# Kernel optimization log

Measured on AMD Instinct MI355X. Metric: run time of the kernel, lower is better.

The kernel has to match this reference:

```python
import jax, jax.numpy as jnp
import numpy as np

B, L, H = 512, 50, 256
N_NODE, N_CATE, N_REL, DEG = 200000, 1000, 4, 12
N = B * L          # graph nodes (seed items of the neighbor-sampled subgraph)
E = N * DEG        # sampled edges (12 neighbors per seed node)


def _layer_norm(x):
    # CARES.layer_norm: center then divide by L2 norm of the centered vector
    x = x - jnp.mean(x, -1, keepdims=True)
    return x / jnp.sqrt(jnp.sum(x * x, -1, keepdims=True))


def _ave_pool(h, gm):
    # h: [B,L,H], gm: [B,L] float
    return jnp.sum(h * gm[..., None], 1) / jnp.sum(gm, 1)[:, None]


def _session_encoder(Ws, bs, w5, Wt, bt, seq_hidden, mean_item, mean_cate, mask):
    # Ws: [4,H,H], bs: [4,H], w5: [H], Wt: [2H,H], bt: [H]
    b, l, h = seq_hidden.shape
    last = (jnp.sum(mask, 1) - 1)[:, None, None]
    ht = jnp.take_along_axis(seq_hidden, jnp.broadcast_to(last, (b, 1, h)), axis=1)[:, 0]
    q1 = (ht @ Ws[0] + bs[0])[:, None, :]
    q2 = (mean_item @ Ws[1] + bs[1])[:, None, :]
    q3 = seq_hidden @ Ws[2] + bs[2]
    q4 = (mean_cate @ Ws[3] + bs[3])[:, None, :]
    alpha = jnp.einsum('blh,h->bl', jax.nn.sigmoid(q1 + q2 + q3 + q4), w5)[..., None]
    a = jnp.sum(alpha * seq_hidden * mask[..., None].astype(seq_hidden.dtype), 1)
    return jnp.concatenate([a, ht], 1) @ Wt + bt


def _gat(x, edge_index, rel_e, edge_attr, gat_W, n_nodes):
    # relation-aware single-head GAT layer: gather -> edge attention -> segment softmax -> scatter
    h = x @ gat_W                               # [N,H]
    src, dst = edge_index[0], edge_index[1]
    msg = h[src] + rel_e                        # [E,H] relation-augmented message
    logit = jax.nn.leaky_relu(jnp.sum(h[dst] * msg, -1) / np.sqrt(h.shape[-1]).astype(np.float32), 0.2) + edge_attr
    mx = jax.ops.segment_max(logit, dst, num_segments=n_nodes)
    ex = jnp.exp(logit - mx[dst])
    den = jax.ops.segment_sum(ex, dst, num_segments=n_nodes)
    att = ex / (den[dst] + 1e-12)
    return jax.ops.segment_sum(att[:, None] * msg, dst, num_segments=n_nodes)


def setup_inputs() -> dict:
    key = jax.random.key(0)
    ks = jax.random.split(key, 20)
    s = 1.0 / np.sqrt(H)  # reset_parameters: uniform(-stdv, stdv)
    uni = lambda k, shape: jax.random.uniform(k, shape, jnp.float32, -s, s)
    return {
        'alias_inputs': jax.random.randint(ks[0], (B, L), 0, L),
        'items': jax.random.randint(ks[1], (B, L), 1, N_NODE),
        'mask': jnp.ones((B, L), jnp.int32),
        'cates': jax.random.randint(ks[2], (B, L), 0, N_CATE),
        'edge_index': jax.random.randint(ks[3], (2, E), 0, N),
        'edge_type': jax.random.randint(ks[4], (E,), 0, N_REL),
        'edge_attr': jax.random.normal(ks[5], (E,), jnp.float32) * 0.1,
        'item_emb': uni(ks[6], (N_NODE, H)),
        'cate_emb': uni(ks[7], (N_CATE, H)),
        'pos_emb': uni(ks[8], (L, H)),
        'len_emb': uni(ks[9], (2 * L, H)),
        'rel_emb': uni(ks[10], (N_REL, H)),
        'se_W': uni(ks[11], (2, 4, H, H)),   # linears one..four for the 2 SessionEncoders
        'se_b': uni(ks[12], (2, 4, H)),
        'se_w5': uni(ks[13], (2, H)),        # linear_five (H->1, no bias)
        'se_Wt': uni(ks[14], (2, 2 * H, H)), # linear_transform
        'se_bt': uni(ks[15], (2, H)),
        'gat_W': uni(ks[16], (H, H)),
    }


def reference(alias_inputs, items, mask, cates, edge_index, edge_type, edge_attr,
              item_emb, cate_emb, pos_emb, len_emb, rel_emb,
              se_W, se_b, se_w5, se_Wt, se_bt, gat_W):
    gm = jnp.sign(items).astype(jnp.float32)            # graph_mask
    hidden = item_emb[items]                            # [B,L,H]
    cate_hidden = cate_emb[cates]
    mean_item = _ave_pool(hidden, gm)
    mean_cate = _ave_pool(cate_hidden, gm)

    # h0 = hidden[i][alias_inputs[i]]
    idx = jnp.broadcast_to(alias_inputs[..., None], (B, L, H))
    h0 = jnp.take_along_axis(hidden, idx, axis=1)

    # add_pos_encoding
    pos = jnp.arange(L - 1, -1, -1)[None, :]
    len_d = jnp.sum(mask, 1, keepdims=True)             # [B,1]
    pos_index = (pos - (L - len_d)) * mask              # [B,L]
    seq_hidden = h0 + pos_emb[pos_index] + len_emb[jnp.broadcast_to(len_d, (B, L))]

    local_sess = _session_encoder(se_W[0], se_b[0], se_w5[0], se_Wt[0], se_bt[0],
                                  seq_hidden, mean_item, mean_cate, mask)

    # relation-aware GAT over the sampled subgraph
    x = item_emb[items.reshape(-1)]                     # [N,H]
    out = _gat(x, edge_index, rel_emb[edge_type], edge_attr, gat_W, N)
    graph_emb = out.reshape(B, L, H)
    s_node = _ave_pool(graph_emb, gm)

    g_seq = jnp.take_along_axis(graph_emb, idx, axis=1)
    global_sess = _session_encoder(se_W[1], se_b[1], se_w5[1], se_Wt[1], se_bt[1],
                                   g_seq, mean_item, s_node, mask)

    return _layer_norm(local_sess + global_sess)        # [B,H]
```

## Files before the change

kernel.cpp:

```cpp
#include <hip/hip_runtime.h>

#define B 512
#define L 50
#define H 256
#define GN (B*L)
#define GE (GN*12)

__device__ __forceinline__ float waveSum(float v){
  #pragma unroll
  for (int m=32;m>0;m>>=1) v += __shfl_xor(v, m, 64);
  return v;
}
__device__ __forceinline__ float sigm(float x){ return 1.f/(1.f+expf(-x)); }

__global__ void k_gather_means(const int* items, const int* cates, const int* mask,
                               const float* item_emb, const float* cate_emb,
                               float* hidden, float* mi, float* mc, float* gms, int* lend){
  int b=blockIdx.x, h=threadIdx.x;
  float si=0.f, sc=0.f, g=0.f; int lm=0;
  for (int l=0;l<L;l++){
    int it=items[b*L+l];
    float gm=(it>0)?1.f:((it<0)?-1.f:0.f);
    float v=item_emb[(size_t)it*H+h];
    hidden[((size_t)b*L+l)*H+h]=v;
    si += gm*v;
    sc += gm*cate_emb[(size_t)cates[b*L+l]*H+h];
    g += gm;
    lm += mask[b*L+l];
  }
  mi[(size_t)b*H+h]=si/g; mc[(size_t)b*H+h]=sc/g;
  if (h==0){ gms[b]=g; lend[b]=lm; }
}

__global__ void k_seq(const int* alias_, const int* mask, const float* hidden,
                      const float* pos_emb, const float* len_emb, const int* lend,
                      float* seqh, float* ht){
  int r=blockIdx.x, lane=threadIdx.x;
  int b=r/L, l=r%L;
  int a=alias_[r];
  int ld=lend[b];
  int m=mask[r];
  int pidx=(ld-1-l)*m;
  if (pidx<0) pidx+=L;
  float4 hv=*reinterpret_cast<const float4*>(hidden+((size_t)b*L+a)*H+lane*4);
  float4 pv=*reinterpret_cast<const float4*>(pos_emb+(size_t)pidx*H+lane*4);
  float4 lv=*reinterpret_cast<const float4*>(len_emb+(size_t)ld*H+lane*4);
  float4 o=make_float4(hv.x+pv.x+lv.x, hv.y+pv.y+lv.y, hv.z+pv.z+lv.z, hv.w+pv.w+lv.w);
  *reinterpret_cast<float4*>(seqh+(size_t)r*H+lane*4)=o;
  if (l == (ld+L-1)%L)
    *reinterpret_cast<float4*>(ht+(size_t)b*H+lane*4)=o;
}

__global__ __launch_bounds__(256) void k_gemm(const float* A, const float* W, size_t wOff,
                                              float* C, const float* bias, size_t bOff,
                                              int M, int Nc, int K){
  __shared__ float At[16][68];
  __shared__ float Ws[16][64];
  int bm=blockIdx.x*64, bn=blockIdx.y*64;
  int t=threadIdx.x;
  int tx=t&15, ty=t>>4;
  float c[4][4]={};
  int r=t>>2, kq=(t&3)<<2;
  int kk=t>>4, nq=(t&15)<<2;
  for (int k0=0;k0<K;k0+=16){
    float4 av=*reinterpret_cast<const float4*>(A+(size_t)(bm+r)*K+(k0+kq));
    At[kq+0][r]=av.x; At[kq+1][r]=av.y; At[kq+2][r]=av.z; At[kq+3][r]=av.w;
    float4 wv=*reinterpret_cast<const float4*>(W+wOff+(size_t)(k0+kk)*Nc+(bn+nq));
    Ws[kk][nq+0]=wv.x; Ws[kk][nq+1]=wv.y; Ws[kk][nq+2]=wv.z; Ws[kk][nq+3]=wv.w;
    __syncthreads();
    #pragma unroll
    for (int q=0;q<16;q++){
      float4 a4=*reinterpret_cast<const float4*>(&At[q][ty<<2]);
      float4 w4=*reinterpret_cast<const float4*>(&Ws[q][tx<<2]);
      float aa[4]={a4.x,a4.y,a4.z,a4.w};
      float ww[4]={w4.x,w4.y,w4.z,w4.w};
      #pragma unroll
      for (int i=0;i<4;i++)
        #pragma unroll
        for (int j=0;j<4;j++) c[i][j]=fmaf(aa[i],ww[j],c[i][j]);
    }
    __syncthreads();
  }
  #pragma unroll
  for (int i=0;i<4;i++){
    size_t row=(size_t)(bm+(ty<<2)+i);
    #pragma unroll
    for (int j=0;j<4;j++){
      int col=bn+(tx<<2)+j;
      float v=c[i][j];
      if (bias) v+=bias[bOff+col];
      C[row*Nc+col]=v;
    }
  }
}

__global__ __launch_bounds__(256) void k_qb3(const float* A0, const float* A1, const float* A2,
                                             const float* W, size_t wBase,
                                             const float* seb, size_t bOff, float* C){
  __shared__ float At[16][68];
  __shared__ float Ws[16][64];
  int bm=blockIdx.x*64, bn=blockIdx.y*64;
  int t=threadIdx.x;
  int tx=t&15, ty=t>>4;
  float c[4][4]={};
  int r=t>>2, kq=(t&3)<<2;
  int kk=t>>4, nq=(t&15)<<2;
  const float* As[3]={A0,A1,A2};
  const int widx[3]={0,1,3};
  for (int src=0;src<3;src++){
    const float* A=As[src];
    size_t wOff=wBase+(size_t)widx[src]*H*H;
    for (int k0=0;k0<H;k0+=16){
      float4 av=*reinterpret_cast<const float4*>(A+(size_t)(bm+r)*H+(k0+kq));
      At[kq+0][r]=av.x; At[kq+1][r]=av.y; At[kq+2][r]=av.z; At[kq+3][r]=av.w;
      float4 wv=*reinterpret_cast<const float4*>(W+wOff+(size_t)(k0+kk)*H+(bn+nq));
      Ws[kk][nq+0]=wv.x; Ws[kk][nq+1]=wv.y; Ws[kk][nq+2]=wv.z; Ws[kk][nq+3]=wv.w;
      __syncthreads();
      #pragma unroll
      for (int q=0;q<16;q++){
        float4 a4=*reinterpret_cast<const float4*>(&At[q][ty<<2]);
        float4 w4=*reinterpret_cast<const float4*>(&Ws[q][tx<<2]);
        float aa[4]={a4.x,a4.y,a4.z,a4.w};
        float ww[4]={w4.x,w4.y,w4.z,w4.w};
        #pragma unroll
        for (int i=0;i<4;i++)
          #pragma unroll
          for (int j=0;j<4;j++) c[i][j]=fmaf(aa[i],ww[j],c[i][j]);
      }
      __syncthreads();
    }
  }
  #pragma unroll
  for (int i=0;i<4;i++){
    size_t row=(size_t)(bm+(ty<<2)+i);
    #pragma unroll
    for (int j=0;j<4;j++){
      int col=bn+(tx<<2)+j;
      float v=c[i][j]
        + seb[bOff+0*H+col] + seb[bOff+1*H+col]
        + seb[bOff+2*H+col] + seb[bOff+3*H+col];
      C[row*H+col]=v;
    }
  }
}

__global__ void k_alpha(const float* qb, const float* q3, const float* w5, size_t wOff,
                        float* alpha){
  int gid=blockIdx.x*blockDim.x+threadIdx.x;
  int wid=gid>>6, lane=gid&63;
  if (wid>=GN) return;
  int b=wid/L;
  float4 qv=*reinterpret_cast<const float4*>(qb+(size_t)b*H+lane*4);
  float4 q3v=*reinterpret_cast<const float4*>(q3+(size_t)wid*H+lane*4);
  float4 wv=*reinterpret_cast<const float4*>(w5+wOff+(size_t)lane*4);
  float part = wv.x*sigm(qv.x+q3v.x) + wv.y*sigm(qv.y+q3v.y)
             + wv.z*sigm(qv.z+q3v.z) + wv.w*sigm(qv.w+q3v.w);
  part=waveSum(part);
  if (lane==0) alpha[wid]=part;
}

__global__ void k_pool(const float* alpha, const float* seqh, const int* mask, const float* ht, float* cat){
  int b=blockIdx.x, h=threadIdx.x;
  float a=0.f;
  for (int l=0;l<L;l++)
    a += alpha[b*L+l]*seqh[((size_t)b*L+l)*H+h]*(float)mask[b*L+l];
  cat[(size_t)b*2*H+h]=a;
  cat[(size_t)b*2*H+H+h]=ht[(size_t)b*H+h];
}

__global__ void k_count(const int* dst, int* cnt){
  int e=blockIdx.x*blockDim.x+threadIdx.x;
  if (e<GE) atomicAdd(&cnt[dst[e]],1);
}

__global__ void k_scan(const int* cnt, int* rowp){
  __shared__ int s[1024];
  int t=threadIdx.x;
  int base=t*25;
  int local[25]; int sum=0;
  #pragma unroll
  for (int i=0;i<25;i++){ local[i]=sum; sum+=cnt[base+i]; }
  s[t]=sum; __syncthreads();
  for (int off=1;off<1024;off<<=1){
    int v=(t>=off)?s[t-off]:0; __syncthreads();
    s[t]+=v; __syncthreads();
  }
  int excl=s[t]-sum;
  #pragma unroll
  for (int i=0;i<25;i++) rowp[base+i]=excl+local[i];
  if (t==1023) rowp[GN]=s[1023];
}

__global__ void k_fill(const int* dst, const int* rowp, int* cnt, int* eord){
  int e=blockIdx.x*blockDim.x+threadIdx.x;
  if (e<GE){ int d=dst[e]; int pos=rowp[d]+atomicAdd(&cnt[d],1); eord[pos]=e; }
}

__global__ void k_node(const float* hg, const int* src, const int* etype, const float* eattr,
                       const float* rel, const int* rowp, const int* eord, float* out){
  int gid=blockIdx.x*blockDim.x+threadIdx.x;
  int n=gid>>6, lane=gid&63;
  if (n>=GN) return;
  float4 hn=*reinterpret_cast<const float4*>(hg+(size_t)n*H+lane*4);
  int b0=rowp[n], b1=rowp[n+1];
  float mx=-INFINITY, den=0.f;
  float4 acc=make_float4(0.f,0.f,0.f,0.f);
  for (int i=b0;i<b1;i++){
    int e=eord[i]; int s=src[e]; int ty=etype[e];
    float4 hs=*reinterpret_cast<const float4*>(hg+(size_t)s*H+lane*4);
    float4 rv=*reinterpret_cast<const float4*>(rel+(size_t)ty*H+lane*4);
    float4 m4=make_float4(hs.x+rv.x,hs.y+rv.y,hs.z+rv.z,hs.w+rv.w);
    float p=hn.x*m4.x+hn.y*m4.y+hn.z*m4.z+hn.w*m4.w;
    p=waveSum(p)*(1.f/16.f);
    float lg=(p>0.f?p:0.2f*p)+eattr[e];
    if (lg>mx){
      float sc=expf(mx-lg);
      den*=sc; acc.x*=sc; acc.y*=sc; acc.z*=sc; acc.w*=sc;
      mx=lg;
    }
    float ex=expf(lg-mx);
    den+=ex;
    acc.x+=ex*m4.x; acc.y+=ex*m4.y; acc.z+=ex*m4.z; acc.w+=ex*m4.w;
  }
  float inv=1.f/(den+1e-12f);
  float4 o=make_float4(acc.x*inv,acc.y*inv,acc.z*inv,acc.w*inv);
  *reinterpret_cast<float4*>(out+(size_t)n*H+lane*4)=o;
}

__global__ void k_avepool(const float* x, const int* items, const float* gms, float* out){
  int b=blockIdx.x, h=threadIdx.x;
  float s=0.f;
  for (int l=0;l<L;l++){
    int it=items[b*L+l];
    float gm=(it>0)?1.f:((it<0)?-1.f:0.f);
    s += gm*x[((size_t)b*L+l)*H+h];
  }
  out[(size_t)b*H+h]=s/gms[b];
}

__global__ void k_gseq(const int* alias_, const float* graph, const int* lend, float* gseq, float* ht){
  int r=blockIdx.x, lane=threadIdx.x;
  int b=r/L, l=r%L;
  int a=alias_[r];
  float4 v=*reinterpret_cast<const float4*>(graph+((size_t)b*L+a)*H+lane*4);
  *reinterpret_cast<float4*>(gseq+(size_t)r*H+lane*4)=v;
  int ld=lend[b];
  if (l == (ld+L-1)%L)
    *reinterpret_cast<float4*>(ht+(size_t)b*H+lane*4)=v;
}

__global__ void k_final(const float* sl, const float* sg, float* out){
  __shared__ float red[8];
  int b=blockIdx.x, h=threadIdx.x;
  int wid=h>>6, lane=h&63;
  float v=sl[(size_t)b*H+h]+sg[(size_t)b*H+h];
  float s=waveSum(v);
  if (lane==0) red[wid]=s;
  __syncthreads();
  float tot=red[0]+red[1]+red[2]+red[3];
  float x=v-tot/(float)H;
  float s2=waveSum(x*x);
  __syncthreads();
  if (lane==0) red[wid]=s2;
  __syncthreads();
  float ss=red[0]+red[1]+red[2]+red[3];
  out[(size_t)b*H+h]=x/sqrtf(ss);
}

extern "C" void kernel_launch(void* const* d_in, const int* in_sizes, int n_in,
                              void* d_out, int out_size, void* d_ws, size_t ws_size,
                              hipStream_t stream){
  (void)in_sizes; (void)n_in; (void)out_size; (void)ws_size;
  const int* alias_=(const int*)d_in[0];
  const int* items =(const int*)d_in[1];
  const int* mask  =(const int*)d_in[2];
  const int* cates =(const int*)d_in[3];
  const int* eind  =(const int*)d_in[4];
  const int* etype =(const int*)d_in[5];
  const float* eattr   =(const float*)d_in[6];
  const float* item_emb=(const float*)d_in[7];
  const float* cate_emb=(const float*)d_in[8];
  const float* pos_emb =(const float*)d_in[9];
  const float* len_emb =(const float*)d_in[10];
  const float* rel_emb =(const float*)d_in[11];
  const float* se_W    =(const float*)d_in[12];
  const float* se_b    =(const float*)d_in[13];
  const float* se_w5   =(const float*)d_in[14];
  const float* se_Wt   =(const float*)d_in[15];
  const float* se_bt   =(const float*)d_in[16];
  const float* gat_W   =(const float*)d_in[17];
  const int* esrc=eind; const int* edst=eind+GE;

  char* w=(char*)d_ws;
  auto carve=[&](size_t nbytes)->char*{ char* p=w; w += (nbytes+255)&~(size_t)255; return p; };
  float* buf1 =(float*)carve((size_t)GN*H*4);
  float* buf2 =(float*)carve((size_t)GN*H*4);
  float* hgat =(float*)carve((size_t)GN*H*4);
  float* q3   =(float*)carve((size_t)GN*H*4);
  float* alphaB=(float*)carve((size_t)GN*4);
  float* qb   =(float*)carve((size_t)B*H*4);
  float* mi   =(float*)carve((size_t)B*H*4);
  float* mc   =(float*)carve((size_t)B*H*4);
  float* sn   =(float*)carve((size_t)B*H*4);
  float* gms  =(float*)carve((size_t)B*4);
  int*   lend =(int*)  carve((size_t)B*4);
  float* htb  =(float*)carve((size_t)B*H*4);
  float* htg  =(float*)carve((size_t)B*H*4);
  float* catb =(float*)carve((size_t)B*2*H*4);
  float* sl   =(float*)carve((size_t)B*H*4);
  float* sg   =(float*)carve((size_t)B*H*4);
  int*   cnt  =(int*)  carve((size_t)GN*4);
  int*   rowp =(int*)  carve((size_t)(GN+1)*4);
  int*   eord =(int*)  carve((size_t)GE*4);

  dim3 blk(256), gBig(GN/64,H/64), gSm(B/64,H/64);

  k_gather_means<<<B,256,0,stream>>>(items,cates,mask,item_emb,cate_emb,buf1,mi,mc,gms,lend);
  k_seq<<<GN,64,0,stream>>>(alias_,mask,buf1,pos_emb,len_emb,lend,buf2,htb);

  k_gemm<<<gBig,blk,0,stream>>>(buf1, gat_W, 0, hgat, nullptr,0, GN,H,H);

  k_gemm<<<gBig,blk,0,stream>>>(buf2, se_W, (size_t)2*H*H, q3, nullptr,0, GN,H,H);
  k_qb3<<<gSm,blk,0,stream>>>(htb, mi, mc, se_W, 0, se_b, 0, qb);
  k_alpha<<<GN/4,256,0,stream>>>(qb,q3,se_w5,0,alphaB);
  k_pool<<<B,256,0,stream>>>(alphaB,buf2,mask,htb,catb);
  k_gemm<<<gSm,blk,0,stream>>>(catb, se_Wt, 0, sl, se_bt, 0, B,H,2*H);

  (void)hipMemsetAsync(cnt,0,(size_t)GN*4,stream);
  k_count<<<GE/256,256,0,stream>>>(edst,cnt);
  k_scan<<<1,1024,0,stream>>>(cnt,rowp);
  (void)hipMemsetAsync(cnt,0,(size_t)GN*4,stream);
  k_fill<<<GE/256,256,0,stream>>>(edst,rowp,cnt,eord);
  k_node<<<GN/4,256,0,stream>>>(hgat,esrc,etype,eattr,rel_emb,rowp,eord,buf1);

  k_avepool<<<B,256,0,stream>>>(buf1,items,gms,sn);
  k_gseq<<<GN,64,0,stream>>>(alias_,buf1,lend,buf2,htg);
  k_gemm<<<gBig,blk,0,stream>>>(buf2, se_W, (size_t)6*H*H, q3, nullptr,0, GN,H,H);
  k_qb3<<<gSm,blk,0,stream>>>(htg, mi, sn, se_W, (size_t)4*H*H, se_b, (size_t)4*H, qb);
  k_alpha<<<GN/4,256,0,stream>>>(qb,q3,se_w5,(size_t)H,alphaB);
  k_pool<<<B,256,0,stream>>>(alphaB,buf2,mask,htg,catb);
  k_gemm<<<gSm,blk,0,stream>>>(catb, se_Wt, (size_t)2*H*H, sg, se_bt, (size_t)H, B,H,2*H);

  k_final<<<B,256,0,stream>>>(sl,sg,(float*)d_out);
}
```

Measured before the change: 818.0 us.

## Run the three large GEMMs on bf16 MFMA with pre-transposed weights

Replaces the fp32 scalar tiled GEMM for the three big N×256×256 products with an MFMA bf16 kernel (16x16x32). Producer kernels now also write bf16 copies of their activations, and a small kernel converts and transposes the three weight matrices to bf16 once per call. This moves the dominant GEMM work onto matrix cores and halves its input traffic. In exchange it adds extra bf16 write traffic, a weight-prep launch, and reduced precision in the GEMM inputs.

```diff
diff --git a/kernel.cpp b/kernel.cpp
--- a/kernel.cpp
+++ b/kernel.cpp
@@ -6,6 +6,13 @@
 #define GN (B*L)
 #define GE (GN*12)
 
+typedef unsigned short u16;
+typedef unsigned int u32;
+typedef __attribute__((ext_vector_type(8))) short short8;
+typedef __attribute__((ext_vector_type(8))) unsigned short u16x8;
+typedef __attribute__((ext_vector_type(4))) float f32x4;
+
+__device__ __forceinline__ u16 f2bf(float f){ u32 x=__float_as_uint(f); u32 r=x+0x7FFFu+((x>>16)&1u); return (u16)(r>>16); }
 __device__ __forceinline__ float waveSum(float v){
   #pragma unroll
   for (int m=32;m>0;m>>=1) v += __shfl_xor(v, m, 64);
@@ -15,7 +22,7 @@
 
 __global__ void k_gather_means(const int* items, const int* cates, const int* mask,
                                const float* item_emb, const float* cate_emb,
-                               float* hidden, float* mi, float* mc, float* gms, int* lend){
+                               float* hidden, u16* hiddenBf, float* mi, float* mc, float* gms, int* lend){
   int b=blockIdx.x, h=threadIdx.x;
   float si=0.f, sc=0.f, g=0.f; int lm=0;
   for (int l=0;l<L;l++){
@@ -23,6 +30,7 @@
     float gm=(it>0)?1.f:((it<0)?-1.f:0.f);
     float v=item_emb[(size_t)it*H+h];
     hidden[((size_t)b*L+l)*H+h]=v;
+    hiddenBf[((size_t)b*L+l)*H+h]=f2bf(v);
     si += gm*v;
     sc += gm*cate_emb[(size_t)cates[b*L+l]*H+h];
     g += gm;
@@ -34,7 +42,7 @@
 
 __global__ void k_seq(const int* alias_, const int* mask, const float* hidden,
                       const float* pos_emb, const float* len_emb, const int* lend,
-                      float* seqh, float* ht){
+                      float* seqh, u16* seqBf, float* ht){
   int r=blockIdx.x, lane=threadIdx.x;
   int b=r/L, l=r%L;
   int a=alias_[r];
@@ -47,8 +55,49 @@
   float4 lv=*reinterpret_cast<const float4*>(len_emb+(size_t)ld*H+lane*4);
   float4 o=make_float4(hv.x+pv.x+lv.x, hv.y+pv.y+lv.y, hv.z+pv.z+lv.z, hv.w+pv.w+lv.w);
   *reinterpret_cast<float4*>(seqh+(size_t)r*H+lane*4)=o;
+  ushort4 ob=make_ushort4(f2bf(o.x),f2bf(o.y),f2bf(o.z),f2bf(o.w));
+  *reinterpret_cast<ushort4*>(seqBf+(size_t)r*H+lane*4)=ob;
   if (l == (ld+L-1)%L)
     *reinterpret_cast<float4*>(ht+(size_t)b*H+lane*4)=o;
+}
+
+__global__ void k_prepW(const float* gat_W, const float* se_W, u16* WbfT){
+  int n=blockIdx.x, g=blockIdx.y, k=threadIdx.x;
+  const float* src = (g==0)? gat_W : (g==1? se_W+(size_t)2*H*H : se_W+(size_t)6*H*H);
+  WbfT[((size_t)g*H+n)*H+k] = f2bf(src[(size_t)k*H+n]);
+}
+
+__global__ __launch_bounds__(256) void k_gemm_mfma(const u16* Abf, const u16* WbfT,
+                                                   float* C, int M){
+  __shared__ u16 As[64][40];
+  __shared__ u16 Bs[64][40];
+  int bm=blockIdx.x*64, bn=blockIdx.y*64;
+  int t=threadIdx.x, wv=t>>6, lane=t&63;
+  int sr=t>>2, sk=(t&3)<<3;
+  f32x4 acc[4]={};
+  for (int k0=0;k0<H;k0+=32){
+    u16x8 av=*reinterpret_cast<const u16x8*>(Abf+(size_t)(bm+sr)*H+k0+sk);
+    u16x8 bv=*reinterpret_cast<const u16x8*>(WbfT+(size_t)(bn+sr)*H+k0+sk);
+    *reinterpret_cast<u16x8*>(&As[sr][sk])=av;
+    *reinterpret_cast<u16x8*>(&Bs[sr][sk])=bv;
+    __syncthreads();
+    int row=(wv<<4)+(lane&15);
+    int ks=(lane>>4)<<3;
+    short8 a=*reinterpret_cast<const short8*>(&As[row][ks]);
+    #pragma unroll
+    for (int ns=0;ns<4;ns++){
+      short8 b=*reinterpret_cast<const short8*>(&Bs[(ns<<4)+(lane&15)][ks]);
+      acc[ns]=__builtin_amdgcn_mfma_f32_16x16x32_bf16(a,b,acc[ns],0,0,0);
+    }
+    __syncthreads();
+  }
+  int r0=bm+(wv<<4)+((lane>>4)<<2);
+  int c0=bn+(lane&15);
+  #pragma unroll
+  for (int ns=0;ns<4;ns++)
+    #pragma unroll
+    for (int i=0;i<4;i++)
+      C[(size_t)(r0+i)*H + c0 + (ns<<4)] = acc[ns][i];
 }
 
 __global__ __launch_bounds__(256) void k_gemm(const float* A, const float* W, size_t wOff,
@@ -238,12 +287,15 @@
   out[(size_t)b*H+h]=s/gms[b];
 }
 
-__global__ void k_gseq(const int* alias_, const float* graph, const int* lend, float* gseq, float* ht){
+__global__ void k_gseq(const int* alias_, const float* graph, const int* lend,
+                       float* gseq, u16* gseqBf, float* ht){
   int r=blockIdx.x, lane=threadIdx.x;
   int b=r/L, l=r%L;
   int a=alias_[r];
   float4 v=*reinterpret_cast<const float4*>(graph+((size_t)b*L+a)*H+lane*4);
   *reinterpret_cast<float4*>(gseq+(size_t)r*H+lane*4)=v;
+  ushort4 vb=make_ushort4(f2bf(v.x),f2bf(v.y),f2bf(v.z),f2bf(v.w));
+  *reinterpret_cast<ushort4*>(gseqBf+(size_t)r*H+lane*4)=vb;
   int ld=lend[b];
   if (l == (ld+L-1)%L)
     *reinterpret_cast<float4*>(ht+(size_t)b*H+lane*4)=v;
@@ -297,6 +349,10 @@
   float* buf2 =(float*)carve((size_t)GN*H*4);
   float* hgat =(float*)carve((size_t)GN*H*4);
   float* q3   =(float*)carve((size_t)GN*H*4);
+  u16*   hidBf=(u16*)  carve((size_t)GN*H*2);
+  u16*   seqBf=(u16*)  carve((size_t)GN*H*2);
+  u16*   gsqBf=(u16*)  carve((size_t)GN*H*2);
+  u16*   wbfT =(u16*)  carve((size_t)3*H*H*2);
   float* alphaB=(float*)carve((size_t)GN*4);
   float* qb   =(float*)carve((size_t)B*H*4);
   float* mi   =(float*)carve((size_t)B*H*4);
@@ -313,14 +369,15 @@
   int*   rowp =(int*)  carve((size_t)(GN+1)*4);
   int*   eord =(int*)  carve((size_t)GE*4);
 
-  dim3 blk(256), gBig(GN/64,H/64), gSm(B/64,H/64);
-
-  k_gather_means<<<B,256,0,stream>>>(items,cates,mask,item_emb,cate_emb,buf1,mi,mc,gms,lend);
-  k_seq<<<GN,64,0,stream>>>(alias_,mask,buf1,pos_emb,len_emb,lend,buf2,htb);
-
-  k_gemm<<<gBig,blk,0,stream>>>(buf1, gat_W, 0, hgat, nullptr,0, GN,H,H);
-
-  k_gemm<<<gBig,blk,0,stream>>>(buf2, se_W, (size_t)2*H*H, q3, nullptr,0, GN,H,H);
+  dim3 blk(256), gSm(B/64,H/64), gM(GN/64,H/64), gPrep(H,3);
+
+  k_prepW<<<gPrep,H,0,stream>>>(gat_W, se_W, wbfT);
+  k_gather_means<<<B,256,0,stream>>>(items,cates,mask,item_emb,cate_emb,buf1,hidBf,mi,mc,gms,lend);
+  k_seq<<<GN,64,0,stream>>>(alias_,mask,buf1,pos_emb,len_emb,lend,buf2,seqBf,htb);
+
+  k_gemm_mfma<<<gM,blk,0,stream>>>(hidBf, wbfT, hgat, GN);
+
+  k_gemm_mfma<<<gM,blk,0,stream>>>(seqBf, wbfT+(size_t)1*H*H, q3, GN);
   k_qb3<<<gSm,blk,0,stream>>>(htb, mi, mc, se_W, 0, se_b, 0, qb);
   k_alpha<<<GN/4,256,0,stream>>>(qb,q3,se_w5,0,alphaB);
   k_pool<<<B,256,0,stream>>>(alphaB,buf2,mask,htb,catb);
@@ -334,8 +391,8 @@
   k_node<<<GN/4,256,0,stream>>>(hgat,esrc,etype,eattr,rel_emb,rowp,eord,buf1);
 
   k_avepool<<<B,256,0,stream>>>(buf1,items,gms,sn);
-  k_gseq<<<GN,64,0,stream>>>(alias_,buf1,lend,buf2,htg);
-  k_gemm<<<gBig,blk,0,stream>>>(buf2, se_W, (size_t)6*H*H, q3, nullptr,0, GN,H,H);
+  k_gseq<<<GN,64,0,stream>>>(alias_,buf1,lend,buf2,gsqBf,htg);
+  k_gemm_mfma<<<gM,blk,0,stream>>>(gsqBf, wbfT+(size_t)2*H*H, q3, GN);
   k_qb3<<<gSm,blk,0,stream>>>(htg, mi, sn, se_W, (size_t)4*H*H, se_b, (size_t)4*H, qb);
   k_alpha<<<GN/4,256,0,stream>>>(qb,q3,se_w5,(size_t)H,alphaB);
   k_pool<<<B,256,0,stream>>>(alphaB,buf2,mask,htg,catb);
```

After: 707.9 us. 1.16x faster.
